# Kernel tuning notes

Hardware: AMD Instinct MI355X
Metric: run time of the kernel (lower is better)

The kernel has to match this reference:

```python
import jax, jax.numpy as jnp
import numpy as np


def _rgb_to_hue(x):
    # x: [B, 3, H, W] in [0,1]; returns hue channel [B, H, W] in [0,1),
    # matching skimage.color.rgb2hsv's hue definition.
    r, g, b = x[:, 0], x[:, 1], x[:, 2]
    maxc = jnp.max(x, axis=1)
    minc = jnp.min(x, axis=1)
    delta = maxc - minc
    safe = jnp.where(delta == 0, 1.0, delta)  # avoid div-by-zero
    h = jnp.where(
        maxc == r, (g - b) / safe,
        jnp.where(maxc == g, 2.0 + (b - r) / safe, 4.0 + (r - g) / safe),
    )
    h = jnp.where(delta == 0, 0.0, (h / 6.0) % 1.0)
    return h


def setup_inputs() -> dict:
    key = jax.random.key(0)
    k1, k2 = jax.random.split(key)
    B, C, H, W = 32, 3, 512, 512
    predict = jax.random.uniform(k1, (B, C, H, W), dtype=jnp.float32)
    target = jax.random.uniform(k2, (B, C, H, W), dtype=jnp.float32)
    return {"predict": predict, "target": target}


def reference(predict, target):
    hp = _rgb_to_hue(predict)  # [B, H, W]
    ht = _rgb_to_hue(target)
    diff = jnp.abs(hp - ht)
    mask = (diff > 0.5).astype(diff.dtype)
    mask_ = (diff < 0.5).astype(diff.dtype)
    # mean(|diff*mask_|) + mean(|diff*mask - 0.5*mask|); first term already >= 0
    loss = jnp.mean(diff * mask_) + jnp.mean(jnp.abs((diff - 0.5) * mask))
    return loss
```

## Files before the change

### kernel.cpp

```cpp
#include <hip/hip_runtime.h>

#define HW_PLANE (512 * 512)
#define NPIX     (32 * HW_PLANE)
#define NBLOCKS  2048

__device__ __forceinline__ float hue1(float r, float g, float b) {
    float maxc  = fmaxf(r, fmaxf(g, b));
    float minc  = fminf(r, fminf(g, b));
    float delta = maxc - minc;
    float safe  = (delta == 0.0f) ? 1.0f : delta;
    float rs    = __builtin_amdgcn_rcpf(safe);
    float hr = (g - b) * rs;
    float hg = 2.0f + (b - r) * rs;
    float hb = 4.0f + (r - g) * rs;
    float h  = (maxc == r) ? hr : ((maxc == g) ? hg : hb);
    h = h * (1.0f / 6.0f);
    h = h - floorf(h);
    return (delta == 0.0f) ? 0.0f : h;
}

__device__ __forceinline__ void acc_diff(float hp, float ht, float& lo, float& hi) {
    float d = fabsf(hp - ht);
    if (d < 0.5f)      lo += d;
    else if (d > 0.5f) hi += d - 0.5f;
}

__global__ void __launch_bounds__(256)
hsv_partial(const float* __restrict__ pred, const float* __restrict__ targ,
            float2* __restrict__ partial) {
    const int tid    = blockIdx.x * blockDim.x + threadIdx.x;
    const int stride = gridDim.x * blockDim.x;
    const int N4     = NPIX / 4;

    float lo = 0.0f, hi = 0.0f;
    #pragma unroll 2
    for (int i = tid; i < N4; i += stride) {
        int p    = i << 2;
        int bimg = p >> 18;
        int pix  = p & (HW_PLANE - 1);
        int base = bimg * (3 * HW_PLANE) + pix;

        float4 pr = *(const float4*)(pred + base);
        float4 pg = *(const float4*)(pred + base + HW_PLANE);
        float4 pb = *(const float4*)(pred + base + 2 * HW_PLANE);
        float4 tr = *(const float4*)(targ + base);
        float4 tg = *(const float4*)(targ + base + HW_PLANE);
        float4 tb = *(const float4*)(targ + base + 2 * HW_PLANE);

        acc_diff(hue1(pr.x, pg.x, pb.x), hue1(tr.x, tg.x, tb.x), lo, hi);
        acc_diff(hue1(pr.y, pg.y, pb.y), hue1(tr.y, tg.y, tb.y), lo, hi);
        acc_diff(hue1(pr.z, pg.z, pb.z), hue1(tr.z, tg.z, tb.z), lo, hi);
        acc_diff(hue1(pr.w, pg.w, pb.w), hue1(tr.w, tg.w, tb.w), lo, hi);
    }

    for (int off = 32; off > 0; off >>= 1) {
        lo += __shfl_down(lo, off, 64);
        hi += __shfl_down(hi, off, 64);
    }
    __shared__ float slo[4], shi[4];
    int lane = threadIdx.x & 63;
    int wave = threadIdx.x >> 6;
    if (lane == 0) { slo[wave] = lo; shi[wave] = hi; }
    __syncthreads();
    if (threadIdx.x == 0) {
        partial[blockIdx.x] =
            make_float2(slo[0] + slo[1] + slo[2] + slo[3],
                        shi[0] + shi[1] + shi[2] + shi[3]);
    }
}

__global__ void __launch_bounds__(256)
hsv_final(const float2* __restrict__ partial, float* __restrict__ out, int nblocks) {
    float lo = 0.0f, hi = 0.0f;
    for (int i = threadIdx.x; i < nblocks; i += blockDim.x) {
        float2 p = partial[i];
        lo += p.x; hi += p.y;
    }
    for (int off = 32; off > 0; off >>= 1) {
        lo += __shfl_down(lo, off, 64);
        hi += __shfl_down(hi, off, 64);
    }
    __shared__ float slo[4], shi[4];
    int lane = threadIdx.x & 63;
    int wave = threadIdx.x >> 6;
    if (lane == 0) { slo[wave] = lo; shi[wave] = hi; }
    __syncthreads();
    if (threadIdx.x == 0) {
        float L = slo[0] + slo[1] + slo[2] + slo[3];
        float H = shi[0] + shi[1] + shi[2] + shi[3];
        out[0] = (L + H) * (1.0f / (float)NPIX);
    }
}

extern "C" void kernel_launch(void* const* d_in, const int* in_sizes, int n_in,
                              void* d_out, int out_size, void* d_ws, size_t ws_size,
                              hipStream_t stream) {
    const float* pred = (const float*)d_in[0];
    const float* targ = (const float*)d_in[1];
    float*  out     = (float*)d_out;
    float2* partial = (float2*)d_ws;

    hsv_partial<<<NBLOCKS, 256, 0, stream>>>(pred, targ, partial);
    hsv_final<<<1, 256, 0, stream>>>(partial, out, NBLOCKS);
}
```

Measured before the change: 214.9 us.

## Stage inputs through LDS with async global_load_lds double buffering

Replaces direct float4 global loads with per-wave asynchronous global-to-LDS copies and double buffering across four subtiles, so each block now owns a contiguous tile of pixels instead of using a grid-stride loop. The intent is to keep more memory requests in flight and overlap the loads with the hue computation. It adds LDS traffic, manual vmcnt waits, and relies on the builtin's per-lane LDS addressing being correct. 2048 blocks times 4096 pixels exactly covers all pixels.

```diff
diff --git a/kernel.cpp b/kernel.cpp
--- a/kernel.cpp
+++ b/kernel.cpp
@@ -3,6 +3,16 @@
 #define HW_PLANE (512 * 512)
 #define NPIX     (32 * HW_PLANE)
 #define NBLOCKS  2048
+#define WAVE_PX  256
+#define SUBTILES 4
+#define BLOCK_PX (4 * WAVE_PX * SUBTILES)
+
+typedef __attribute__((address_space(3))) float*       lds_fp;
+typedef const __attribute__((address_space(1))) float* glb_fp;
+
+__device__ __forceinline__ void stage16(const float* g, float* l) {
+    __builtin_amdgcn_global_load_lds((glb_fp)g, (lds_fp)l, 16, 0, 0);
+}
 
 __device__ __forceinline__ float hue1(float r, float g, float b) {
     float maxc  = fmaxf(r, fmaxf(g, b));
@@ -28,25 +38,47 @@
 __global__ void __launch_bounds__(256)
 hsv_partial(const float* __restrict__ pred, const float* __restrict__ targ,
             float2* __restrict__ partial) {
-    const int tid    = blockIdx.x * blockDim.x + threadIdx.x;
-    const int stride = gridDim.x * blockDim.x;
-    const int N4     = NPIX / 4;
+    __shared__ float lds[4 * 2 * 6 * WAVE_PX];
+
+    const int lane = threadIdx.x & 63;
+    const int wave = threadIdx.x >> 6;
+    const int blockpix = blockIdx.x * BLOCK_PX;
+    const int img  = blockpix >> 18;
+    const int pix0 = (blockpix & (HW_PLANE - 1)) + wave * WAVE_PX;
+    const float* pbase = pred + img * (3 * HW_PLANE) + pix0;
+    const float* tbase = targ + img * (3 * HW_PLANE) + pix0;
+
+    float* lbuf[2] = { &lds[(wave * 2 + 0) * 6 * WAVE_PX],
+                       &lds[(wave * 2 + 1) * 6 * WAVE_PX] };
+
+    auto stage = [&](int s, float* lb) {
+        const int off = s * (4 * WAVE_PX) + lane * 4;
+        #pragma unroll
+        for (int c = 0; c < 3; ++c) {
+            stage16(pbase + c * HW_PLANE + off, lb + c       * WAVE_PX + lane * 4);
+            stage16(tbase + c * HW_PLANE + off, lb + (3 + c) * WAVE_PX + lane * 4);
+        }
+    };
+
+    stage(0, lbuf[0]);
 
     float lo = 0.0f, hi = 0.0f;
-    #pragma unroll 2
-    for (int i = tid; i < N4; i += stride) {
-        int p    = i << 2;
-        int bimg = p >> 18;
-        int pix  = p & (HW_PLANE - 1);
-        int base = bimg * (3 * HW_PLANE) + pix;
-
-        float4 pr = *(const float4*)(pred + base);
-        float4 pg = *(const float4*)(pred + base + HW_PLANE);
-        float4 pb = *(const float4*)(pred + base + 2 * HW_PLANE);
-        float4 tr = *(const float4*)(targ + base);
-        float4 tg = *(const float4*)(targ + base + HW_PLANE);
-        float4 tb = *(const float4*)(targ + base + 2 * HW_PLANE);
-
+    #pragma unroll
+    for (int s = 0; s < SUBTILES; ++s) {
+        float* cur = lbuf[s & 1];
+        if (s + 1 < SUBTILES) {
+            stage(s + 1, lbuf[(s + 1) & 1]);
+            asm volatile("s_waitcnt vmcnt(6)" ::: "memory");
+        } else {
+            asm volatile("s_waitcnt vmcnt(0)" ::: "memory");
+        }
+        const float* q = cur + lane * 4;
+        float4 pr = *(const float4*)(q + 0 * WAVE_PX);
+        float4 pg = *(const float4*)(q + 1 * WAVE_PX);
+        float4 pb = *(const float4*)(q + 2 * WAVE_PX);
+        float4 tr = *(const float4*)(q + 3 * WAVE_PX);
+        float4 tg = *(const float4*)(q + 4 * WAVE_PX);
+        float4 tb = *(const float4*)(q + 5 * WAVE_PX);
         acc_diff(hue1(pr.x, pg.x, pb.x), hue1(tr.x, tg.x, tb.x), lo, hi);
         acc_diff(hue1(pr.y, pg.y, pb.y), hue1(tr.y, tg.y, tb.y), lo, hi);
         acc_diff(hue1(pr.z, pg.z, pb.z), hue1(tr.z, tg.z, tb.z), lo, hi);
@@ -58,8 +90,6 @@
         hi += __shfl_down(hi, off, 64);
     }
     __shared__ float slo[4], shi[4];
-    int lane = threadIdx.x & 63;
-    int wave = threadIdx.x >> 6;
     if (lane == 0) { slo[wave] = lo; shi[wave] = hi; }
     __syncthreads();
     if (threadIdx.x == 0) {
```

Measured after the change: 219.3 us. 2.1% more time.
